# Kernel tuning notes

Hardware: AMD Instinct MI355X
Metric: run time of the kernel (lower is better)

## Reference

```python
import jax, jax.numpy as jnp
import numpy as np

B, IN_DIM, OUT_DIM = 4096, 2048, 2048
EMA_M = 0.95
LN_EPS = 1e-5


def setup_inputs() -> dict:
    key = jax.random.key(0)
    ks = jax.random.split(key, 8)
    x = jax.random.normal(ks[0], (B, IN_DIM), dtype=jnp.float32)
    # W_slow is orthogonal-init in torch (gain 0.5); scaled gaussian is a fine stand-in for math testing
    W_slow = jax.random.normal(ks[1], (OUT_DIM, IN_DIM), dtype=jnp.float32) * (0.5 / np.sqrt(IN_DIM))
    # buffers start at zero in torch; use small nonzero values so the medium/fast GEMMs are exercised
    W_medium = jax.random.normal(ks[2], (OUT_DIM, IN_DIM), dtype=jnp.float32) * 0.01
    W_fast = jax.random.normal(ks[3], (OUT_DIM, IN_DIM), dtype=jnp.float32) * 0.01
    ln_gamma = jnp.ones((OUT_DIM,), jnp.float32) + 0.1 * jax.random.normal(ks[4], (OUT_DIM,), dtype=jnp.float32)
    ln_beta = 0.1 * jax.random.normal(ks[5], (OUT_DIM,), dtype=jnp.float32)
    pc_w1 = jax.random.normal(ks[6], (8, 3), dtype=jnp.float32) * 0.5
    pc_b1 = jnp.zeros((8,), jnp.float32)
    pc_w2 = jax.random.normal(ks[7], (1, 8), dtype=jnp.float32) * 0.5
    pc_b2 = jnp.full((1,), -1.5, jnp.float32)  # torch fills last Linear bias with -1.5
    ema_mean = jnp.zeros((1,), jnp.float32)
    ema_std = jnp.ones((1,), jnp.float32)
    return {"x": x, "W_slow": W_slow, "W_medium": W_medium, "W_fast": W_fast,
            "ln_gamma": ln_gamma, "ln_beta": ln_beta,
            "pc_w1": pc_w1, "pc_b1": pc_b1, "pc_w2": pc_w2, "pc_b2": pc_b2,
            "ema_mean": ema_mean, "ema_std": ema_std}


def reference(x, W_slow, W_medium, W_fast, ln_gamma, ln_beta,
              pc_w1, pc_b1, pc_w2, pc_b2, ema_mean, ema_std):
    xc = jnp.clip(x, -5.0, 5.0)
    slow_out = jnp.clip(xc @ W_slow.T, -10.0, 10.0)
    pre_act = jnp.clip(slow_out + xc @ W_medium.T + xc @ W_fast.T, -10.0, 10.0)  # [B, OUT]

    batch_mean = pre_act.mean(axis=1, keepdims=True)                      # [B,1]
    batch_std = jnp.maximum(pre_act.std(axis=1, keepdims=True), 1e-6)     # [B,1], ddof=0

    # EMA buffer update (no-grad in torch); clamps applied after update
    new_mean = jnp.clip(EMA_M * ema_mean + (1.0 - EMA_M) * batch_mean.mean(), -0.5, 0.5)
    new_std = jnp.clip(EMA_M * ema_std + (1.0 - EMA_M) * batch_std.mean(), 0.1, 1.5)
    homeostasis = new_std / (jnp.abs(new_mean) + 1e-6)                    # [1]

    stats = jnp.concatenate([batch_mean, batch_std,
                             jnp.broadcast_to(homeostasis[None, :], (batch_mean.shape[0], 1))], axis=1)  # [B,3]
    h = jax.nn.gelu(stats @ pc_w1.T + pc_b1, approximate=False)           # torch GELU is exact erf
    learned_plasticity = jax.nn.sigmoid(h @ pc_w2.T + pc_b2)[:, 0]        # [B] (does not affect `out`)
    _ = learned_plasticity  # kept for fidelity with original compute graph

    # LayerNorm over last dim, eps=1e-5
    mu = pre_act.mean(axis=-1, keepdims=True)
    var = pre_act.var(axis=-1, keepdims=True)
    normed = (pre_act - mu) * jax.lax.rsqrt(var + LN_EPS) * ln_gamma + ln_beta
    out = 5.0 * jnp.tanh(normed / 5.0)
    return out
```

## Files before the change

kernel.cpp:

```cpp
#include <hip/hip_runtime.h>
#include <hip/hip_bf16.h>

#define BDIM    4096
#define IN_DIM  2048
#define OUT_DIM 2048

typedef __attribute__((ext_vector_type(4))) float  floatx4;
typedef __attribute__((ext_vector_type(8))) short  bf16x8;

__device__ __forceinline__ unsigned short f2bf(float f) {
    union { float f; unsigned u; } v; v.f = f;
    unsigned r = v.u + 0x7FFFu + ((v.u >> 16) & 1u);
    return (unsigned short)(r >> 16);
}

__device__ __forceinline__ void async16(const unsigned short* g, unsigned short* l) {
    __builtin_amdgcn_global_load_lds(
        (const __attribute__((address_space(1))) unsigned int*)g,
        (__attribute__((address_space(3))) unsigned int*)l,
        16, 0, 0);
}

__global__ __launch_bounds__(256) void prep(const float* __restrict__ x,
                                            const float* __restrict__ Ws,
                                            const float* __restrict__ Wm,
                                            const float* __restrict__ Wf,
                                            unsigned short* __restrict__ xc,
                                            unsigned short* __restrict__ bsum) {
    int b = blockIdx.x;
    if (b < 4096) {
        int i0 = b * 512 + threadIdx.x;
#pragma unroll
        for (int r = 0; r < 2; r++) {
            int i = i0 + r * 256;
            float4 v = ((const float4*)x)[i];
            ushort4 o;
            o.x = f2bf(fminf(fmaxf(v.x, -5.f), 5.f));
            o.y = f2bf(fminf(fmaxf(v.y, -5.f), 5.f));
            o.z = f2bf(fminf(fmaxf(v.z, -5.f), 5.f));
            o.w = f2bf(fminf(fmaxf(v.w, -5.f), 5.f));
            ((ushort4*)xc)[i] = o;
        }
    } else {
        int i0 = (b - 4096) * 512 + threadIdx.x;
#pragma unroll
        for (int r = 0; r < 2; r++) {
            int i = i0 + r * 256;
            float4 s = ((const float4*)Ws)[i];
            float4 m = ((const float4*)Wm)[i];
            float4 f = ((const float4*)Wf)[i];
            ushort4 o;
            o.x = f2bf(s.x + m.x + f.x);
            o.y = f2bf(s.y + m.y + f.y);
            o.z = f2bf(s.z + m.z + f.z);
            o.w = f2bf(s.w + m.w + f.w);
            ((ushort4*)bsum)[i] = o;
        }
    }
}

#define TILE  128
#define BK    64
#define ITERS (IN_DIM / BK)

#define MEMBAR() asm volatile("" ::: "memory")

__global__ __launch_bounds__(256, 2) void gemm_bt(const unsigned short* __restrict__ A,
                                                  const unsigned short* __restrict__ B,
                                                  unsigned short* __restrict__ C) {
    constexpr int N = OUT_DIM, K = IN_DIM;
    __shared__ __align__(16) unsigned short As[2 * TILE * BK];
    __shared__ __align__(16) unsigned short Bs[2 * TILE * BK];

    const int tid  = threadIdx.x;
    const int lane = tid & 63;
    const int wave = tid >> 6;
    const int wm   = (wave >> 1) * 64;
    const int wn   = (wave & 1) * 64;
    const int rowBlock = blockIdx.y * TILE;
    const int colBlock = blockIdx.x * TILE;

    const int sRow = tid >> 3;
    const int sSeg = (tid & 7) ^ (sRow & 7);
    const unsigned short* aSrc = A + (size_t)(rowBlock + sRow) * K + sSeg * 8;
    const unsigned short* bSrc = B + (size_t)(colBlock + sRow) * K + sSeg * 8;

    floatx4 acc[4][4] = {};

    const int fragRow = lane & 15;
    const int quad    = lane >> 4;
    const int l7      = lane & 7;

    auto stage = [&](int t, int p) {
        unsigned short* ad = As + p * TILE * BK + tid * 8;
        unsigned short* bd = Bs + p * TILE * BK + tid * 8;
        const unsigned short* ag = aSrc + t * BK;
        const unsigned short* bg = bSrc + t * BK;
#pragma unroll
        for (int r = 0; r < 4; r++)
            async16(ag + (size_t)(r * 32) * K, ad + r * 32 * BK);
#pragma unroll
        for (int r = 0; r < 4; r++)
            async16(bg + (size_t)(r * 32) * K, bd + r * 32 * BK);
    };

    stage(0, 0);
    stage(1, 1);
    __builtin_amdgcn_s_waitcnt(0xF78);
    MEMBAR();
    __builtin_amdgcn_s_barrier();
    MEMBAR();

    for (int k = 0; k < ITERS; k++) {
        const int p = k & 1;
        const unsigned short* Ab = As + p * TILE * BK;
        const unsigned short* Bb = Bs + p * TILE * BK;

#pragma unroll
        for (int kk = 0; kk < 2; kk++) {
            const int xs = ((quad + kk * 4) ^ l7) << 3;
            bf16x8 af[4], bfr[4];
#pragma unroll
            for (int i = 0; i < 4; i++) {
                af[i]  = *(const bf16x8*)(Ab + (wm + i * 16 + fragRow) * BK + xs);
                bfr[i] = *(const bf16x8*)(Bb + (wn + i * 16 + fragRow) * BK + xs);
            }
#pragma unroll
            for (int i = 0; i < 4; i++)
#pragma unroll
                for (int j = 0; j < 4; j++)
                    acc[i][j] = __builtin_amdgcn_mfma_f32_16x16x32_bf16(af[i], bfr[j], acc[i][j], 0, 0, 0);
        }

        MEMBAR();
        __builtin_amdgcn_s_barrier();
        MEMBAR();
        if (k < ITERS - 2) {
            stage(k + 2, p);
            __builtin_amdgcn_s_waitcnt(0xF78);
        } else {
            __builtin_amdgcn_s_waitcnt(0xF70);
        }
        MEMBAR();
        __builtin_amdgcn_s_barrier();
        MEMBAR();
    }

    const int cCol = colBlock + wn + (lane & 15);
    const int cRow = rowBlock + wm + (lane >> 4) * 4;
#pragma unroll
    for (int i = 0; i < 4; i++) {
#pragma unroll
        for (int j = 0; j < 4; j++) {
            const int col = cCol + j * 16;
            const int rb  = cRow + i * 16;
#pragma unroll
            for (int r = 0; r < 4; r++)
                C[(size_t)(rb + r) * N + col] = f2bf(acc[i][j][r]);
        }
    }
}

__global__ __launch_bounds__(256) void ln_kernel(const unsigned short* __restrict__ C,
                                                 const float* __restrict__ gamma,
                                                 const float* __restrict__ beta,
                                                 float* __restrict__ out) {
    const int lane = threadIdx.x & 63;
    const int row  = blockIdx.x * 4 + (threadIdx.x >> 6);
    const uint4* Cr = (const uint4*)(C + (size_t)row * OUT_DIM);

    float v[4][8];
    float sum = 0.f, sq = 0.f;
#pragma unroll
    for (int it = 0; it < 4; it++) {
        uint4 u = Cr[lane + 64 * it];
        unsigned w[4] = { u.x, u.y, u.z, u.w };
#pragma unroll
        for (int e = 0; e < 4; e++) {
            union { unsigned u; float f; } lo, hi;
            lo.u = w[e] << 16;
            hi.u = w[e] & 0xFFFF0000u;
            float a = fminf(fmaxf(lo.f, -10.f), 10.f);
            float b = fminf(fmaxf(hi.f, -10.f), 10.f);
            v[it][2 * e]     = a;
            v[it][2 * e + 1] = b;
            sum += a + b;
            sq  += a * a + b * b;
        }
    }
#pragma unroll
    for (int off = 32; off > 0; off >>= 1) {
        sum += __shfl_xor(sum, off);
        sq  += __shfl_xor(sq,  off);
    }
    const float mu  = sum * (1.0f / OUT_DIM);
    const float var = sq * (1.0f / OUT_DIM) - mu * mu;
    const float inv = rsqrtf(var + 1e-5f);

    float* orow = out + (size_t)row * OUT_DIM;
#pragma unroll
    for (int it = 0; it < 4; it++) {
        const int base = (lane + 64 * it) * 8;
        float4 g0 = *(const float4*)(gamma + base);
        float4 g1 = *(const float4*)(gamma + base + 4);
        float4 b0 = *(const float4*)(beta + base);
        float4 b1 = *(const float4*)(beta + base + 4);
        float4 o0, o1;
        float z;
        z = (v[it][0] - mu) * inv * g0.x + b0.x; o0.x = 5.f * (1.f - 2.f / (__expf(0.4f * z) + 1.f));
        z = (v[it][1] - mu) * inv * g0.y + b0.y; o0.y = 5.f * (1.f - 2.f / (__expf(0.4f * z) + 1.f));
        z = (v[it][2] - mu) * inv * g0.z + b0.z; o0.z = 5.f * (1.f - 2.f / (__expf(0.4f * z) + 1.f));
        z = (v[it][3] - mu) * inv * g0.w + b0.w; o0.w = 5.f * (1.f - 2.f / (__expf(0.4f * z) + 1.f));
        z = (v[it][4] - mu) * inv * g1.x + b1.x; o1.x = 5.f * (1.f - 2.f / (__expf(0.4f * z) + 1.f));
        z = (v[it][5] - mu) * inv * g1.y + b1.y; o1.y = 5.f * (1.f - 2.f / (__expf(0.4f * z) + 1.f));
        z = (v[it][6] - mu) * inv * g1.z + b1.z; o1.z = 5.f * (1.f - 2.f / (__expf(0.4f * z) + 1.f));
        z = (v[it][7] - mu) * inv * g1.w + b1.w; o1.w = 5.f * (1.f - 2.f / (__expf(0.4f * z) + 1.f));
        *(float4*)(orow + base)     = o0;
        *(float4*)(orow + base + 4) = o1;
    }
}

extern "C" void kernel_launch(void* const* d_in, const int* in_sizes, int n_in,
                              void* d_out, int out_size, void* d_ws, size_t ws_size,
                              hipStream_t stream) {
    const float* x     = (const float*)d_in[0];
    const float* Ws    = (const float*)d_in[1];
    const float* Wm    = (const float*)d_in[2];
    const float* Wf    = (const float*)d_in[3];
    const float* gamma = (const float*)d_in[4];
    const float* beta  = (const float*)d_in[5];
    float* out = (float*)d_out;

    char* ws = (char*)d_ws;
    unsigned short* xc   = (unsigned short*)ws;
    unsigned short* bsum = (unsigned short*)(ws + (size_t)16 * 1024 * 1024);
    unsigned short* Cbuf = (unsigned short*)(ws + (size_t)24 * 1024 * 1024);

    prep<<<6144, 256, 0, stream>>>(x, Ws, Wm, Wf, xc, bsum);
    dim3 g(OUT_DIM / TILE, BDIM / TILE);
    gemm_bt<<<g, 256, 0, stream>>>(xc, bsum, Cbuf);
    ln_kernel<<<BDIM / 4, 256, 0, stream>>>(Cbuf, gamma, beta, out);
}
```

Measured before the change: 185.8 us.

## Fuse prep, GEMM and LayerNorm into one cooperative kernel with grid syncs

```diff
diff --git a/kernel.cpp b/kernel.cpp
--- a/kernel.cpp
+++ b/kernel.cpp
@@ -1,5 +1,8 @@
 #include <hip/hip_runtime.h>
 #include <hip/hip_bf16.h>
+#include <hip/hip_cooperative_groups.h>
+
+namespace cg = cooperative_groups;
 
 #define BDIM    4096
 #define IN_DIM  2048
@@ -7,6 +10,12 @@
 
 typedef __attribute__((ext_vector_type(4))) float  floatx4;
 typedef __attribute__((ext_vector_type(8))) short  bf16x8;
+
+#define TILE  128
+#define BK    64
+#define ITERS (IN_DIM / BK)
+
+#define MEMBAR() asm volatile("" ::: "memory")
 
 __device__ __forceinline__ unsigned short f2bf(float f) {
     union { float f; unsigned u; } v; v.f = f;
@@ -21,15 +30,16 @@
         16, 0, 0);
 }
 
-__global__ __launch_bounds__(256) void prep(const float* __restrict__ x,
-                                            const float* __restrict__ Ws,
-                                            const float* __restrict__ Wm,
-                                            const float* __restrict__ Wf,
-                                            unsigned short* __restrict__ xc,
-                                            unsigned short* __restrict__ bsum) {
-    int b = blockIdx.x;
-    if (b < 4096) {
-        int i0 = b * 512 + threadIdx.x;
+
+__device__ __forceinline__ void prep_chunk(int cid, int tid,
+                                           const float* __restrict__ x,
+                                           const float* __restrict__ Ws,
+                                           const float* __restrict__ Wm,
+                                           const float* __restrict__ Wf,
+                                           unsigned short* __restrict__ xc,
+                                           unsigned short* __restrict__ bsum) {
+    if (cid < 4096) {
+        int i0 = cid * 512 + tid;
 #pragma unroll
         for (int r = 0; r < 2; r++) {
             int i = i0 + r * 256;
@@ -42,7 +52,7 @@
             ((ushort4*)xc)[i] = o;
         }
     } else {
-        int i0 = (b - 4096) * 512 + threadIdx.x;
+        int i0 = (cid - 4096) * 512 + tid;
 #pragma unroll
         for (int r = 0; r < 2; r++) {
             int i = i0 + r * 256;
@@ -59,26 +69,16 @@
     }
 }
 
-#define TILE  128
-#define BK    64
-#define ITERS (IN_DIM / BK)
-
-#define MEMBAR() asm volatile("" ::: "memory")
-
-__global__ __launch_bounds__(256, 2) void gemm_bt(const unsigned short* __restrict__ A,
-                                                  const unsigned short* __restrict__ B,
-                                                  unsigned short* __restrict__ C) {
+__device__ __forceinline__ void gemm_tile(const unsigned short* __restrict__ A,
+                                          const unsigned short* __restrict__ B,
+                                          unsigned short* __restrict__ C,
+                                          unsigned short* As, unsigned short* Bs,
+                                          int rowBlock, int colBlock, int tid) {
     constexpr int N = OUT_DIM, K = IN_DIM;
-    __shared__ __align__(16) unsigned short As[2 * TILE * BK];
-    __shared__ __align__(16) unsigned short Bs[2 * TILE * BK];
-
-    const int tid  = threadIdx.x;
     const int lane = tid & 63;
     const int wave = tid >> 6;
     const int wm   = (wave >> 1) * 64;
     const int wn   = (wave & 1) * 64;
-    const int rowBlock = blockIdx.y * TILE;
-    const int colBlock = blockIdx.x * TILE;
 
     const int sRow = tid >> 3;
     const int sSeg = (tid & 7) ^ (sRow & 7);
@@ -161,12 +161,11 @@
     }
 }
 
-__global__ __launch_bounds__(256) void ln_kernel(const unsigned short* __restrict__ C,
-                                                 const float* __restrict__ gamma,
-                                                 const float* __restrict__ beta,
-                                                 float* __restrict__ out) {
-    const int lane = threadIdx.x & 63;
-    const int row  = blockIdx.x * 4 + (threadIdx.x >> 6);
+__device__ __forceinline__ void ln_row(int row, int lane,
+                                       const unsigned short* __restrict__ C,
+                                       const float* __restrict__ gamma,
+                                       const float* __restrict__ beta,
+                                       float* __restrict__ out) {
     const uint4* Cr = (const uint4*)(C + (size_t)row * OUT_DIM);
 
     float v[4][8];
@@ -181,11 +180,11 @@
             lo.u = w[e] << 16;
             hi.u = w[e] & 0xFFFF0000u;
             float a = fminf(fmaxf(lo.f, -10.f), 10.f);
-            float b = fminf(fmaxf(hi.f, -10.f), 10.f);
+            float bb = fminf(fmaxf(hi.f, -10.f), 10.f);
             v[it][2 * e]     = a;
-            v[it][2 * e + 1] = b;
-            sum += a + b;
-            sq  += a * a + b * b;
+            v[it][2 * e + 1] = bb;
+            sum += a + bb;
+            sq  += a * a + bb * bb;
         }
     }
 #pragma unroll
@@ -220,6 +219,65 @@
     }
 }
 
+__global__ __launch_bounds__(256, 2) void fused(const float* __restrict__ x,
+                                                const float* __restrict__ Ws,
+                                                const float* __restrict__ Wm,
+                                                const float* __restrict__ Wf,
+                                                const float* __restrict__ gamma,
+                                                const float* __restrict__ beta,
+                                                unsigned short* __restrict__ xc,
+                                                unsigned short* __restrict__ bsum,
+                                                unsigned short* __restrict__ Cbuf,
+                                                float* __restrict__ out) {
+    __shared__ __align__(16) unsigned short As[2 * TILE * BK];
+    __shared__ __align__(16) unsigned short Bs[2 * TILE * BK];
+    cg::grid_group grid = cg::this_grid();
+    const int b   = blockIdx.x;
+    const int tid = threadIdx.x;
+
+#pragma unroll
+    for (int c = 0; c < 12; c++)
+        prep_chunk(b + c * 512, tid, x, Ws, Wm, Wf, xc, bsum);
+
+    __threadfence();
+    grid.sync();
+
+    gemm_tile(xc, bsum, Cbuf, As, Bs, (b >> 4) * TILE, (b & 15) * TILE, tid);
+
+    __threadfence();
+    grid.sync();
+
+    const int lane = tid & 63;
+    const int wave = tid >> 6;
+#pragma unroll
+    for (int r2 = 0; r2 < 2; r2++)
+        ln_row(b * 8 + r2 * 4 + wave, lane, Cbuf, gamma, beta, out);
+}
+
+__global__ __launch_bounds__(256) void prep(const float* __restrict__ x,
+                                            const float* __restrict__ Ws,
+                                            const float* __restrict__ Wm,
+                                            const float* __restrict__ Wf,
+                                            unsigned short* __restrict__ xc,
+                                            unsigned short* __restrict__ bsum) {
+    prep_chunk(blockIdx.x, threadIdx.x, x, Ws, Wm, Wf, xc, bsum);
+}
+
+__global__ __launch_bounds__(256, 2) void gemm_bt(const unsigned short* __restrict__ A,
+                                                  const unsigned short* __restrict__ B,
+                                                  unsigned short* __restrict__ C) {
+    __shared__ __align__(16) unsigned short As[2 * TILE * BK];
+    __shared__ __align__(16) unsigned short Bs[2 * TILE * BK];
+    gemm_tile(A, B, C, As, Bs, blockIdx.y * TILE, blockIdx.x * TILE, threadIdx.x);
+}
+
+__global__ __launch_bounds__(256) void ln_kernel(const unsigned short* __restrict__ C,
+                                                 const float* __restrict__ gamma,
+                                                 const float* __restrict__ beta,
+                                                 float* __restrict__ out) {
+    ln_row(blockIdx.x * 4 + (threadIdx.x >> 6), threadIdx.x & 63, C, gamma, beta, out);
+}
+
 extern "C" void kernel_launch(void* const* d_in, const int* in_sizes, int n_in,
                               void* d_out, int out_size, void* d_ws, size_t ws_size,
                               hipStream_t stream) {
@@ -236,8 +294,15 @@
     unsigned short* bsum = (unsigned short*)(ws + (size_t)16 * 1024 * 1024);
     unsigned short* Cbuf = (unsigned short*)(ws + (size_t)24 * 1024 * 1024);
 
-    prep<<<6144, 256, 0, stream>>>(x, Ws, Wm, Wf, xc, bsum);
-    dim3 g(OUT_DIM / TILE, BDIM / TILE);
-    gemm_bt<<<g, 256, 0, stream>>>(xc, bsum, Cbuf);
-    ln_kernel<<<BDIM / 4, 256, 0, stream>>>(Cbuf, gamma, beta, out);
-}
+    void* args[] = { (void*)&x, (void*)&Ws, (void*)&Wm, (void*)&Wf,
+                     (void*)&gamma, (void*)&beta,
+                     (void*)&xc, (void*)&bsum, (void*)&Cbuf, (void*)&out };
+    hipError_t err = hipLaunchCooperativeKernel(reinterpret_cast<void*>(fused),
+                                                dim3(512), dim3(256), args, 0, stream);
+    if (err != hipSuccess) {
+        prep<<<6144, 256, 0, stream>>>(x, Ws, Wm, Wf, xc, bsum);
+        dim3 g(OUT_DIM / TILE, BDIM / TILE);
+        gemm_bt<<<g, 256, 0, stream>>>(xc, bsum, Cbuf);
+        ln_kernel<<<BDIM / 4, 256, 0, stream>>>(Cbuf, gamma, beta, out);
+    }
+}
```

Measured after the change: 465.7 us. 151% more time.

## Enlarge GEMM tile to 128x256 with 512 threads and triple-buffered LDS

Applied to the files above, without the earlier changes.

```diff
diff --git a/kernel.cpp b/kernel.cpp
--- a/kernel.cpp
+++ b/kernel.cpp
@@ -7,6 +7,13 @@
 
 typedef __attribute__((ext_vector_type(4))) float  floatx4;
 typedef __attribute__((ext_vector_type(8))) short  bf16x8;
+
+#define TILE_M 128
+#define TILE_N 256
+#define BK     64
+#define ITERS  (IN_DIM / BK)
+
+#define MEMBAR() asm volatile("" ::: "memory")
 
 __device__ __forceinline__ unsigned short f2bf(float f) {
     union { float f; unsigned u; } v; v.f = f;
@@ -59,26 +66,22 @@
     }
 }
 
-#define TILE  128
-#define BK    64
-#define ITERS (IN_DIM / BK)
-
-#define MEMBAR() asm volatile("" ::: "memory")
-
-__global__ __launch_bounds__(256, 2) void gemm_bt(const unsigned short* __restrict__ A,
+__global__ __launch_bounds__(512, 2) void gemm_bt(const unsigned short* __restrict__ A,
                                                   const unsigned short* __restrict__ B,
                                                   unsigned short* __restrict__ C) {
     constexpr int N = OUT_DIM, K = IN_DIM;
-    __shared__ __align__(16) unsigned short As[2 * TILE * BK];
-    __shared__ __align__(16) unsigned short Bs[2 * TILE * BK];
+    constexpr int AELEMS = TILE_M * BK;
+    constexpr int BELEMS = TILE_N * BK;
+    __shared__ __align__(16) unsigned short As[3 * AELEMS];
+    __shared__ __align__(16) unsigned short Bs[3 * BELEMS];
 
     const int tid  = threadIdx.x;
     const int lane = tid & 63;
     const int wave = tid >> 6;
-    const int wm   = (wave >> 1) * 64;
-    const int wn   = (wave & 1) * 64;
-    const int rowBlock = blockIdx.y * TILE;
-    const int colBlock = blockIdx.x * TILE;
+    const int wm   = (wave >> 2) * 64;
+    const int wn   = (wave & 3) * 64;
+    const int rowBlock = blockIdx.y * TILE_M;
+    const int colBlock = blockIdx.x * TILE_N;
 
     const int sRow = tid >> 3;
     const int sSeg = (tid & 7) ^ (sRow & 7);
@@ -92,29 +95,34 @@
     const int l7      = lane & 7;
 
     auto stage = [&](int t, int p) {
-        unsigned short* ad = As + p * TILE * BK + tid * 8;
-        unsigned short* bd = Bs + p * TILE * BK + tid * 8;
+        unsigned short* ad = As + p * AELEMS + tid * 8;
+        unsigned short* bd = Bs + p * BELEMS + tid * 8;
         const unsigned short* ag = aSrc + t * BK;
         const unsigned short* bg = bSrc + t * BK;
 #pragma unroll
+        for (int r = 0; r < 2; r++)
+            async16(ag + (size_t)(r * 64) * K, ad + r * 4096);
+#pragma unroll
         for (int r = 0; r < 4; r++)
-            async16(ag + (size_t)(r * 32) * K, ad + r * 32 * BK);
-#pragma unroll
-        for (int r = 0; r < 4; r++)
-            async16(bg + (size_t)(r * 32) * K, bd + r * 32 * BK);
+            async16(bg + (size_t)(r * 64) * K, bd + r * 4096);
     };
 
     stage(0, 0);
     stage(1, 1);
-    __builtin_amdgcn_s_waitcnt(0xF78);
+    __builtin_amdgcn_s_waitcnt(0xF76);
     MEMBAR();
     __builtin_amdgcn_s_barrier();
     MEMBAR();
 
+    int pc = 0;
     for (int k = 0; k < ITERS; k++) {
-        const int p = k & 1;
-        const unsigned short* Ab = As + p * TILE * BK;
-        const unsigned short* Bb = Bs + p * TILE * BK;
+        if (k < ITERS - 2) {
+            int ps = pc + 2; if (ps >= 3) ps -= 3;
+            stage(k + 2, ps);
+        }
+
+        const unsigned short* Ab = As + pc * AELEMS;
+        const unsigned short* Bb = Bs + pc * BELEMS;
 
 #pragma unroll
         for (int kk = 0; kk < 2; kk++) {
@@ -136,14 +144,15 @@
         __builtin_amdgcn_s_barrier();
         MEMBAR();
         if (k < ITERS - 2) {
-            stage(k + 2, p);
-            __builtin_amdgcn_s_waitcnt(0xF78);
+            __builtin_amdgcn_s_waitcnt(0xF76);
         } else {
             __builtin_amdgcn_s_waitcnt(0xF70);
         }
         MEMBAR();
         __builtin_amdgcn_s_barrier();
         MEMBAR();
+
+        pc = pc + 1; if (pc == 3) pc = 0;
     }
 
     const int cCol = colBlock + wn + (lane & 15);
@@ -237,7 +246,7 @@
     unsigned short* Cbuf = (unsigned short*)(ws + (size_t)24 * 1024 * 1024);
 
     prep<<<6144, 256, 0, stream>>>(x, Ws, Wm, Wf, xc, bsum);
-    dim3 g(OUT_DIM / TILE, BDIM / TILE);
-    gemm_bt<<<g, 256, 0, stream>>>(xc, bsum, Cbuf);
+    dim3 g(OUT_DIM / TILE_N, BDIM / TILE_M);
+    gemm_bt<<<g, 512, 0, stream>>>(xc, bsum, Cbuf);
     ln_kernel<<<BDIM / 4, 256, 0, stream>>>(Cbuf, gamma, beta, out);
 }
```

Result: slower. 196.5 us (+5.8%).
